# Performance work log

Hardware: AMD Instinct MI355X
Metric: run time of the kernel (lower is better)

The kernel has to match this reference:

```python
import jax, jax.numpy as jnp
import numpy as np

B, EMBED, HIDDEN, NH, D, H, W = 8, 384, 512, 32, 12, 32, 32  # attn_size D = EMBED // NH
SCALE = float(D) ** -0.5


def conv1x1(x, Wm, b):
    # 1x1 conv == per-pixel linear: x (B,Cin,H,W), Wm (Cout,Cin), b (Cout,)
    return jnp.einsum('bchw,oc->bohw', x, Wm) + b[None, :, None, None]


def mha(qc, kc, vc):
    # qc/kc/vc: (B, EMBED, H, W); tokens = H*W, heads = NH, head_dim = D
    HW = H * W
    def split(t):
        return t.reshape(B, NH, D, HW).transpose(0, 1, 3, 2)  # (B, nh, HW, d)
    q = split(qc) * SCALE
    k = split(kc)
    v = split(vc)
    w = jax.nn.softmax(jnp.einsum('bhnd,bhmd->bhnm', q, k), axis=-1)  # (B,nh,HW,HW)
    f = jnp.einsum('bhnm,bhmd->bhnd', w, v)  # (B,nh,HW,d)
    # (B,nh,HW,d) -> (B,HW,nh,d) -> (B,H,W,C) -> (B,C,H,W), matching torch view
    return f.transpose(0, 2, 1, 3).reshape(B, H, W, NH * D).transpose(0, 3, 1, 2)


def setup_inputs() -> dict:
    key = jax.random.key(0)
    ks = jax.random.split(key, 18)
    def p(k, shape):
        return jax.random.normal(k, shape, dtype=jnp.float32) * 0.02
    return {
        'x': jax.random.normal(ks[0], (B, EMBED, H, W), dtype=jnp.float32),
        'x_bpf': jax.random.normal(ks[1], (B, EMBED, H, W), dtype=jnp.float32),
        'Wq': p(ks[2], (EMBED, EMBED)), 'bq': p(ks[3], (EMBED,)),
        'Wk': p(ks[4], (EMBED, EMBED)), 'bk': p(ks[5], (EMBED,)),
        'Wv': p(ks[6], (EMBED, EMBED)), 'bv': p(ks[7], (EMBED,)),
        'Wq_bpf': p(ks[8], (EMBED, EMBED)), 'bq_bpf': p(ks[9], (EMBED,)),
        'Wk_bpf': p(ks[10], (EMBED, EMBED)), 'bk_bpf': p(ks[11], (EMBED,)),
        'Wv_bpf': p(ks[12], (EMBED, EMBED)), 'bv_bpf': p(ks[13], (EMBED,)),
        'Wo': p(ks[14], (HIDDEN, 2 * EMBED)), 'bo': p(ks[15], (HIDDEN,)),
    }


def reference(x, x_bpf, Wq, bq, Wk, bk, Wv, bv, Wq_bpf, bq_bpf, Wk_bpf, bk_bpf, Wv_bpf, bv_bpf, Wo, bo):
    q = conv1x1(x, Wq, bq)
    k = conv1x1(x, Wk, bk)
    v = conv1x1(x, Wv, bv)
    q_bpf = conv1x1(x_bpf, Wq_bpf, bq_bpf)
    k_bpf = conv1x1(x_bpf, Wk_bpf, bk_bpf)
    v_bpf = conv1x1(x_bpf, Wv_bpf, bv_bpf)
    # branch 1: query from bpf stream, key/value from x stream, residual to x
    f = mha(q_bpf, k, v) + x
    # branch 2: query from x stream, key/value from bpf stream, residual to x_bpf
    f_bpf = mha(q, k_bpf, v_bpf) + x_bpf
    fused = jnp.concatenate([f, f_bpf], axis=1)  # (B, 2*EMBED, H, W)
    return conv1x1(fused, Wo, bo)  # (B, HIDDEN, H, W)
```

## Files before the change

kernel.cpp:

```cpp
#include <hip/hip_runtime.h>
#include <hip/hip_bf16.h>

#define BB 8
#define EMBED 384
#define NH 32
#define HD 12
#define HWN 1024
#define HIDDEN 512
#define KTOT 1536
#define SCALE 0.28867513459481287f

typedef __attribute__((ext_vector_type(8))) unsigned short ushort8;
typedef __attribute__((ext_vector_type(8))) short short8;
typedef __attribute__((ext_vector_type(4))) float f32x4;
typedef __attribute__((ext_vector_type(16))) float f32x16;
typedef __attribute__((ext_vector_type(4))) unsigned short ushort4v;
typedef __attribute__((ext_vector_type(2))) unsigned int uint2v;

static __device__ __forceinline__ float bf2f(unsigned short u) {
    return __uint_as_float(((unsigned int)u) << 16);
}
static __device__ __forceinline__ unsigned short f2bf(float f) {
    unsigned int u = __float_as_uint(f);
    u = u + 0x7FFFu + ((u >> 16) & 1u);
    return (unsigned short)(u >> 16);
}
static __device__ __forceinline__ unsigned int cvt_pk_bf16(float lo, float hi) {
    unsigned int r;
    asm("v_cvt_pk_bf16_f32 %0, %1, %2" : "=v"(r) : "v"(lo), "v"(hi));
    return r;
}

struct WConv {
    const float* src[7];
    unsigned short* dst[7];
    int start[8];
};

__global__ __launch_bounds__(256) void k_bf16_all(WConv wc) {
    int i = blockIdx.x * 256 + threadIdx.x;
    if (i >= wc.start[7]) return;
    int p = 0;
#pragma unroll
    for (int j = 1; j < 7; ++j) p += (i >= wc.start[j]);
    const int e = i - wc.start[p];
    const f32x4 v = reinterpret_cast<const f32x4*>(wc.src[p])[e];
    ushort4v o;
#pragma unroll
    for (int j = 0; j < 4; ++j) o[j] = f2bf(v[j]);
    if (p == 6) {
        const int row = e / 192, cc = e % 192;
        ushort4v* d = reinterpret_cast<ushort4v*>(wc.dst[6]);
        d[row * 384 + cc] = o;
        d[row * 384 + 192 + cc] = o;
    } else {
        reinterpret_cast<ushort4v*>(wc.dst[p])[e] = o;
    }
}

__global__ __launch_bounds__(256) void k_transpose(const float* __restrict__ x0, const float* __restrict__ x1,
                                                   unsigned short* __restrict__ fused2) {
    __shared__ float tile[32][33];
    const int z = blockIdx.z;
    const int s = z >> 3, b = z & 7;
    const float* src = (s ? x1 : x0) + (size_t)b * EMBED * HWN;
    unsigned short* dst = fused2 + (size_t)b * HWN * KTOT + 768 + s * 384;
    const int c0 = blockIdx.x * 32;
    const int n0 = blockIdx.y * 32;
    const int tc = threadIdx.x & 31;
    const int tr = threadIdx.x >> 5;
#pragma unroll
    for (int p = 0; p < 4; ++p) {
        int r = tr + p * 8;
        tile[r][tc] = src[(size_t)(c0 + r) * HWN + n0 + tc];
    }
    __syncthreads();
#pragma unroll
    for (int p = 0; p < 4; ++p) {
        int r = tr + p * 8;
        dst[(size_t)(n0 + r) * KTOT + c0 + tc] = f2bf(tile[tc][r]);
    }
}

template <bool F32OUT>
static __device__ __forceinline__ void gemm_core(const unsigned short* __restrict__ A, int lda,
                                                 const unsigned short* __restrict__ Bt, int ldb,
                                                 const float* __restrict__ bias,
                                                 unsigned short* __restrict__ outBf,
                                                 float* __restrict__ outF,
                                                 int K, int bx, int by) {
    __shared__ unsigned short As[64][72];
    __shared__ unsigned short Bs[64][72];
    const int t = threadIdx.x;
    const int lane = t & 63;
    const int wid = t >> 6;
    const int wr = wid >> 1, wc = wid & 1;
    const int o0 = bx * 64, n0 = by * 64;
    const int lrow = t >> 2;
    const int lseg = t & 3;

    f32x4 acc[2][2] = {};

    for (int k0 = 0; k0 < K; k0 += 64) {
        const ushort8* ga = reinterpret_cast<const ushort8*>(A + (size_t)(o0 + lrow) * lda + k0 + lseg * 16);
        const ushort8* gb = reinterpret_cast<const ushort8*>(Bt + (size_t)(n0 + lrow) * ldb + k0 + lseg * 16);
        ushort8 a0 = ga[0], a1 = ga[1];
        ushort8 b0 = gb[0], b1 = gb[1];
        *reinterpret_cast<ushort8*>(&As[lrow][lseg * 16]) = a0;
        *reinterpret_cast<ushort8*>(&As[lrow][lseg * 16 + 8]) = a1;
        *reinterpret_cast<ushort8*>(&Bs[lrow][lseg * 16]) = b0;
        *reinterpret_cast<ushort8*>(&Bs[lrow][lseg * 16 + 8]) = b1;
        __syncthreads();
#pragma unroll
        for (int kk = 0; kk < 2; ++kk) {
            const int ko = kk * 32 + ((lane >> 4) << 3);
            short8 af[2], bfv[2];
            af[0]  = *reinterpret_cast<const short8*>(&As[wr * 32 + (lane & 15)][ko]);
            af[1]  = *reinterpret_cast<const short8*>(&As[wr * 32 + 16 + (lane & 15)][ko]);
            bfv[0] = *reinterpret_cast<const short8*>(&Bs[wc * 32 + (lane & 15)][ko]);
            bfv[1] = *reinterpret_cast<const short8*>(&Bs[wc * 32 + 16 + (lane & 15)][ko]);
#pragma unroll
            for (int i = 0; i < 2; ++i)
#pragma unroll
                for (int j = 0; j < 2; ++j)
                    acc[i][j] = __builtin_amdgcn_mfma_f32_16x16x32_bf16(af[i], bfv[j], acc[i][j], 0, 0, 0);
        }
        __syncthreads();
    }
#pragma unroll
    for (int i = 0; i < 2; ++i) {
#pragma unroll
        for (int j = 0; j < 2; ++j) {
            const int ob = o0 + wr * 32 + i * 16 + ((lane >> 4) << 2);
            const int n  = n0 + wc * 32 + j * 16 + (lane & 15);
#pragma unroll
            for (int r = 0; r < 4; ++r) {
                const int o = ob + r;
                float v = acc[i][j][r] + bias[o];
                if constexpr (F32OUT) outF[(size_t)o * HWN + n] = v;
                else                  outBf[(size_t)o * HWN + n] = f2bf(v);
            }
        }
    }
}

struct QkvTable {
    const unsigned short* W[6];
    const float* bias[6];
    const unsigned short* fused2;
    unsigned short* out[6];
};

__global__ __launch_bounds__(256) void k_gemm_qkv(QkvTable tab) {
    const int z = blockIdx.z;
    const int b = z / 6, p = z % 6;
    const unsigned short* Bt = tab.fused2 + (size_t)b * HWN * KTOT + 768 + (p / 3) * 384;
    gemm_core<false>(tab.W[p], EMBED, Bt, KTOT, tab.bias[p],
                     tab.out[p] + (size_t)b * EMBED * HWN, nullptr,
                     EMBED, blockIdx.x, blockIdx.y);
}

__global__ __launch_bounds__(256) void k_gemm_out(const unsigned short* __restrict__ Wo2,
                                                  const unsigned short* __restrict__ fused2,
                                                  const float* __restrict__ bo,
                                                  float* __restrict__ out) {
    const int b = blockIdx.z;
    gemm_core<true>(Wo2, KTOT, fused2 + (size_t)b * HWN * KTOT, KTOT, bo,
                    nullptr, out + (size_t)b * HIDDEN * HWN,
                    KTOT, blockIdx.x, blockIdx.y);
}

__global__ __launch_bounds__(256) void k_attn_mfma(const unsigned short* __restrict__ qc,
                                                   const unsigned short* __restrict__ kc,
                                                   const unsigned short* __restrict__ vc,
                                                   const unsigned short* __restrict__ qcb,
                                                   const unsigned short* __restrict__ kcb,
                                                   const unsigned short* __restrict__ vcb,
                                                   unsigned short* __restrict__ fused2) {
    __shared__ unsigned short Ks[512][18];
    __shared__ unsigned short Vs[13][520];

    const int bid = blockIdx.x;
    const int inst = bid >> 3, qt = bid & 7;
    const int branch = inst >> 8, b = (inst >> 5) & 7, h = inst & 31;
    const unsigned short* Qg = branch ? qc : qcb;
    const unsigned short* Kg = branch ? kcb : kc;
    const unsigned short* Vg = branch ? vcb : vc;
    const int coff = branch ? 384 : 0;
    const size_t base = ((size_t)b * EMBED + h * HD) * HWN;
    const int t = threadIdx.x;
    const int lane = t & 63, w = t >> 6;
    const int q31 = lane & 31, hi = lane >> 5;
    const int n0 = qt * 128;
    const float C2 = SCALE * 1.4426950408889634f;

    short8 qf = {};
    {
        const int qg = n0 + w * 32 + q31;
#pragma unroll
        for (int j = 0; j < 8; ++j) {
            const int d = hi * 8 + j;
            if (d < HD)
                qf[j] = (short)f2bf(bf2f(Qg[base + (size_t)d * HWN + qg]) * C2);
        }
    }

    f32x16 acc, z16;
#pragma unroll
    for (int r = 0; r < 16; ++r) { acc[r] = 0.f; z16[r] = 0.f; }
    const int vrow = (q31 < HD) ? q31 : 12;

    for (int phase = 0; phase < 2; ++phase) {
        const int m0 = phase << 9;
        __syncthreads();
        {
            const size_t kb = base + (size_t)(4 * w) * HWN + m0;
#pragma unroll
            for (int it = 0; it < 8; ++it) {
                const int m = it * 64 + lane;
                unsigned int da = 0, db = 0;
                if (w < 3) {
                    da = (unsigned int)Kg[kb + m] | ((unsigned int)Kg[kb + HWN + m] << 16);
                    db = (unsigned int)Kg[kb + 2 * HWN + m] | ((unsigned int)Kg[kb + 3 * HWN + m] << 16);
                }
                unsigned int* p = reinterpret_cast<unsigned int*>(&Ks[m][w * 4]);
                p[0] = da;
                p[1] = db;
            }
        }
        if (w < 3) {
#pragma unroll
            for (int r = 0; r < 4; ++r) {
                const int d = 4 * w + r;
                *reinterpret_cast<ushort8*>(&Vs[d][lane * 8]) =
                    *reinterpret_cast<const ushort8*>(&Vg[base + (size_t)d * HWN + m0 + lane * 8]);
            }
        } else {
            ushort8 ones;
#pragma unroll
            for (int j = 0; j < 8; ++j) ones[j] = 0x3F80;
            *reinterpret_cast<ushort8*>(&Vs[12][lane * 8]) = ones;
        }
        __syncthreads();

        for (int mc = 0; mc < 16; ++mc) {
            const int mb = mc << 5;
            union { short8 v; unsigned int u[4]; } kf;
            {
                const unsigned int* kp = reinterpret_cast<const unsigned int*>(&Ks[mb + q31][hi * 8]);
                kf.u[0] = kp[0]; kf.u[1] = kp[1]; kf.u[2] = kp[2]; kf.u[3] = kp[3];
            }
            union { short8 v; uint2v u2[2]; } vf1, vf2;
            vf1.u2[0] = *reinterpret_cast<const uint2v*>(&Vs[vrow][mb + hi * 4]);
            vf1.u2[1] = *reinterpret_cast<const uint2v*>(&Vs[vrow][mb + 8 + hi * 4]);
            vf2.u2[0] = *reinterpret_cast<const uint2v*>(&Vs[vrow][mb + 16 + hi * 4]);
            vf2.u2[1] = *reinterpret_cast<const uint2v*>(&Vs[vrow][mb + 24 + hi * 4]);
            const f32x16 s = __builtin_amdgcn_mfma_f32_32x32x16_bf16(kf.v, qf, z16, 0, 0, 0);
            union { short8 v; unsigned int u[4]; } p1, p2;
#pragma unroll
            for (int r = 0; r < 4; ++r) {
                p1.u[r] = cvt_pk_bf16(__builtin_amdgcn_exp2f(s[2 * r]),
                                      __builtin_amdgcn_exp2f(s[2 * r + 1]));
                p2.u[r] = cvt_pk_bf16(__builtin_amdgcn_exp2f(s[8 + 2 * r]),
                                      __builtin_amdgcn_exp2f(s[8 + 2 * r + 1]));
            }
            acc = __builtin_amdgcn_mfma_f32_32x32x16_bf16(p1.v, vf1.v, acc, 0, 0, 0);
            acc = __builtin_amdgcn_mfma_f32_32x32x16_bf16(p2.v, vf2.v, acc, 0, 0, 0);
        }
    }

    float invq[16];
#pragma unroll
    for (int r = 0; r < 16; ++r)
        invq[r] = 1.0f / __shfl(acc[r], (lane & 32) | 12);

    __syncthreads();
    unsigned short* OtW = &Ks[0][0] + w * 384;
    if (q31 < HD) {
#pragma unroll
        for (int r2 = 0; r2 < 8; ++r2) {
            const int r = 2 * r2;
            const int q = (r & 3) + 8 * (r >> 2) + 4 * hi;
            const unsigned int dw = (unsigned int)f2bf(acc[r] * invq[r]) |
                                    ((unsigned int)f2bf(acc[r + 1] * invq[r + 1]) << 16);
            *reinterpret_cast<unsigned int*>(&OtW[q31 * 32 + q]) = dw;
        }
    }
    __syncthreads();
    {
        const int q = t >> 1, half = t & 1;
        const unsigned short* Osrc = &Ks[0][0] + (q >> 5) * 384 + (half * 6) * 32 + (q & 31);
        const unsigned int w0 = (unsigned int)Osrc[0]   | ((unsigned int)Osrc[32]  << 16);
        const unsigned int w1 = (unsigned int)Osrc[64]  | ((unsigned int)Osrc[96]  << 16);
        const unsigned int w2 = (unsigned int)Osrc[128] | ((unsigned int)Osrc[160] << 16);
        unsigned int* dst = reinterpret_cast<unsigned int*>(
            fused2 + ((size_t)b * HWN + n0 + q) * KTOT + coff + h * HD + half * 6);
        dst[0] = w0; dst[1] = w1; dst[2] = w2;
    }
}

extern "C" void kernel_launch(void* const* d_in, const int* in_sizes, int n_in,
                              void* d_out, int out_size, void* d_ws, size_t ws_size,
                              hipStream_t stream) {
    (void)in_sizes; (void)n_in; (void)out_size; (void)ws_size;
    const float* x   = (const float*)d_in[0];
    const float* xbp = (const float*)d_in[1];
    const float* Wq  = (const float*)d_in[2];  const float* bq  = (const float*)d_in[3];
    const float* Wk  = (const float*)d_in[4];  const float* bk  = (const float*)d_in[5];
    const float* Wv  = (const float*)d_in[6];  const float* bv  = (const float*)d_in[7];
    const float* Wqb = (const float*)d_in[8];  const float* bqb = (const float*)d_in[9];
    const float* Wkb = (const float*)d_in[10]; const float* bkb = (const float*)d_in[11];
    const float* Wvb = (const float*)d_in[12]; const float* bvb = (const float*)d_in[13];
    const float* Wo  = (const float*)d_in[14]; const float* bo  = (const float*)d_in[15];
    float* out = (float*)d_out;

    char* ws = (char*)d_ws;
    size_t off = 0;
    auto alloc = [&](size_t bytes) -> void* {
        void* p = ws + off;
        off = (off + bytes + 255) & ~(size_t)255;
        return p;
    };
    unsigned short* wbf[6];
    for (int i = 0; i < 6; ++i) wbf[i] = (unsigned short*)alloc((size_t)EMBED * EMBED * 2);
    unsigned short* wo2 = (unsigned short*)alloc((size_t)HIDDEN * KTOT * 2);
    unsigned short* qkv[6];
    for (int i = 0; i < 6; ++i) qkv[i] = (unsigned short*)alloc((size_t)BB * EMBED * HWN * 2);
    unsigned short* fused2 = (unsigned short*)alloc((size_t)BB * HWN * KTOT * 2);

    WConv wc;
    const float* wsrc[7] = {Wq, Wk, Wv, Wqb, Wkb, Wvb, Wo};
    unsigned short* wdst[7] = {wbf[0], wbf[1], wbf[2], wbf[3], wbf[4], wbf[5], wo2};
    int acc4 = 0;
    for (int i = 0; i < 7; ++i) {
        const int n = (i < 6) ? EMBED * EMBED : HIDDEN * 768;
        wc.src[i] = wsrc[i];
        wc.dst[i] = wdst[i];
        wc.start[i] = acc4;
        acc4 += n / 4;
    }
    wc.start[7] = acc4;
    k_bf16_all<<<(acc4 + 255) / 256, 256, 0, stream>>>(wc);

    k_transpose<<<dim3(EMBED / 32, HWN / 32, 16), 256, 0, stream>>>(x, xbp, fused2);

    QkvTable tab;
    tab.W[0] = wbf[0]; tab.W[1] = wbf[1]; tab.W[2] = wbf[2];
    tab.W[3] = wbf[3]; tab.W[4] = wbf[4]; tab.W[5] = wbf[5];
    tab.bias[0] = bq; tab.bias[1] = bk; tab.bias[2] = bv;
    tab.bias[3] = bqb; tab.bias[4] = bkb; tab.bias[5] = bvb;
    tab.fused2 = fused2;
    for (int i = 0; i < 6; ++i) tab.out[i] = qkv[i];
    k_gemm_qkv<<<dim3(EMBED / 64, HWN / 64, BB * 6), 256, 0, stream>>>(tab);

    k_attn_mfma<<<dim3(4096), 256, 0, stream>>>(qkv[0], qkv[1], qkv[2], qkv[3], qkv[4], qkv[5],
                                                fused2);

    k_gemm_out<<<dim3(HIDDEN / 64, HWN / 64, BB), 256, 0, stream>>>(wo2, fused2, bo, out);
}
```

Measured before the change: 166.4 us.

## Process two query tiles per attention block to reuse staged K/V

Each attention block now handles 256 queries instead of 128 by keeping two Q fragments and two accumulators per wave. The K/V tiles staged in shared memory are reused across both, which halves the total K/V global loads and staging work, and the grid drops from 4096 to 2048 blocks. Block indexing is also reordered so consecutive blocks map to different head instances rather than query tiles of the same head. The cost is higher register pressure, possibly lower occupancy, and fewer blocks to spread across the GPU. The output transpose staging uses a padded stride so eight sub-tiles fit in the existing shared buffer.

```diff
diff --git a/kernel.cpp b/kernel.cpp
--- a/kernel.cpp
+++ b/kernel.cpp
@@ -170,6 +170,7 @@
                     KTOT, blockIdx.x, blockIdx.y);
 }
 
+#define OT_STRIDE 416
 __global__ __launch_bounds__(256) void k_attn_mfma(const unsigned short* __restrict__ qc,
                                                    const unsigned short* __restrict__ kc,
                                                    const unsigned short* __restrict__ vc,
@@ -181,7 +182,7 @@
     __shared__ unsigned short Vs[13][520];
 
     const int bid = blockIdx.x;
-    const int inst = bid >> 3, qt = bid & 7;
+    const int inst = bid & 511, qt = bid >> 9;
     const int branch = inst >> 8, b = (inst >> 5) & 7, h = inst & 31;
     const unsigned short* Qg = branch ? qc : qcb;
     const unsigned short* Kg = branch ? kcb : kc;
@@ -191,23 +192,24 @@
     const int t = threadIdx.x;
     const int lane = t & 63, w = t >> 6;
     const int q31 = lane & 31, hi = lane >> 5;
-    const int n0 = qt * 128;
+    const int n0 = qt * 256;
     const float C2 = SCALE * 1.4426950408889634f;
 
-    short8 qf = {};
-    {
-        const int qg = n0 + w * 32 + q31;
+    short8 qf[2] = {};
+#pragma unroll
+    for (int i = 0; i < 2; ++i) {
+        const int qg = n0 + i * 128 + w * 32 + q31;
 #pragma unroll
         for (int j = 0; j < 8; ++j) {
             const int d = hi * 8 + j;
             if (d < HD)
-                qf[j] = (short)f2bf(bf2f(Qg[base + (size_t)d * HWN + qg]) * C2);
-        }
-    }
-
-    f32x16 acc, z16;
-#pragma unroll
-    for (int r = 0; r < 16; ++r) { acc[r] = 0.f; z16[r] = 0.f; }
+                qf[i][j] = (short)f2bf(bf2f(Qg[base + (size_t)d * HWN + qg]) * C2);
+        }
+    }
+
+    f32x16 acc[2], z16;
+#pragma unroll
+    for (int r = 0; r < 16; ++r) { acc[0][r] = 0.f; acc[1][r] = 0.f; z16[r] = 0.f; }
     const int vrow = (q31 < HD) ? q31 : 12;
 
     for (int phase = 0; phase < 2; ++phase) {
@@ -255,47 +257,59 @@
             vf1.u2[1] = *reinterpret_cast<const uint2v*>(&Vs[vrow][mb + 8 + hi * 4]);
             vf2.u2[0] = *reinterpret_cast<const uint2v*>(&Vs[vrow][mb + 16 + hi * 4]);
             vf2.u2[1] = *reinterpret_cast<const uint2v*>(&Vs[vrow][mb + 24 + hi * 4]);
-            const f32x16 s = __builtin_amdgcn_mfma_f32_32x32x16_bf16(kf.v, qf, z16, 0, 0, 0);
-            union { short8 v; unsigned int u[4]; } p1, p2;
-#pragma unroll
-            for (int r = 0; r < 4; ++r) {
-                p1.u[r] = cvt_pk_bf16(__builtin_amdgcn_exp2f(s[2 * r]),
-                                      __builtin_amdgcn_exp2f(s[2 * r + 1]));
-                p2.u[r] = cvt_pk_bf16(__builtin_amdgcn_exp2f(s[8 + 2 * r]),
-                                      __builtin_amdgcn_exp2f(s[8 + 2 * r + 1]));
-            }
-            acc = __builtin_amdgcn_mfma_f32_32x32x16_bf16(p1.v, vf1.v, acc, 0, 0, 0);
-            acc = __builtin_amdgcn_mfma_f32_32x32x16_bf16(p2.v, vf2.v, acc, 0, 0, 0);
-        }
-    }
-
-    float invq[16];
-#pragma unroll
-    for (int r = 0; r < 16; ++r)
-        invq[r] = 1.0f / __shfl(acc[r], (lane & 32) | 12);
+#pragma unroll
+            for (int i = 0; i < 2; ++i) {
+                const f32x16 s = __builtin_amdgcn_mfma_f32_32x32x16_bf16(kf.v, qf[i], z16, 0, 0, 0);
+                union { short8 v; unsigned int u[4]; } p1, p2;
+#pragma unroll
+                for (int r = 0; r < 4; ++r) {
+                    p1.u[r] = cvt_pk_bf16(__builtin_amdgcn_exp2f(s[2 * r]),
+                                          __builtin_amdgcn_exp2f(s[2 * r + 1]));
+                    p2.u[r] = cvt_pk_bf16(__builtin_amdgcn_exp2f(s[8 + 2 * r]),
+                                          __builtin_amdgcn_exp2f(s[8 + 2 * r + 1]));
+                }
+                acc[i] = __builtin_amdgcn_mfma_f32_32x32x16_bf16(p1.v, vf1.v, acc[i], 0, 0, 0);
+                acc[i] = __builtin_amdgcn_mfma_f32_32x32x16_bf16(p2.v, vf2.v, acc[i], 0, 0, 0);
+            }
+        }
+    }
+
+    float invq[2][16];
+#pragma unroll
+    for (int i = 0; i < 2; ++i)
+#pragma unroll
+        for (int r = 0; r < 16; ++r)
+            invq[i][r] = 1.0f / __shfl(acc[i][r], (lane & 32) | 12);
 
     __syncthreads();
-    unsigned short* OtW = &Ks[0][0] + w * 384;
-    if (q31 < HD) {
-#pragma unroll
-        for (int r2 = 0; r2 < 8; ++r2) {
-            const int r = 2 * r2;
-            const int q = (r & 3) + 8 * (r >> 2) + 4 * hi;
-            const unsigned int dw = (unsigned int)f2bf(acc[r] * invq[r]) |
-                                    ((unsigned int)f2bf(acc[r + 1] * invq[r + 1]) << 16);
-            *reinterpret_cast<unsigned int*>(&OtW[q31 * 32 + q]) = dw;
+#pragma unroll
+    for (int i = 0; i < 2; ++i) {
+        unsigned short* OtW = &Ks[0][0] + (i * 4 + w) * OT_STRIDE;
+        if (q31 < HD) {
+#pragma unroll
+            for (int r2 = 0; r2 < 8; ++r2) {
+                const int r = 2 * r2;
+                const int q = (r & 3) + 8 * (r >> 2) + 4 * hi;
+                const unsigned int dw = (unsigned int)f2bf(acc[i][r] * invq[i][r]) |
+                                        ((unsigned int)f2bf(acc[i][r + 1] * invq[i][r + 1]) << 16);
+                *reinterpret_cast<unsigned int*>(&OtW[q31 * 32 + q]) = dw;
+            }
         }
     }
     __syncthreads();
     {
-        const int q = t >> 1, half = t & 1;
-        const unsigned short* Osrc = &Ks[0][0] + (q >> 5) * 384 + (half * 6) * 32 + (q & 31);
-        const unsigned int w0 = (unsigned int)Osrc[0]   | ((unsigned int)Osrc[32]  << 16);
-        const unsigned int w1 = (unsigned int)Osrc[64]  | ((unsigned int)Osrc[96]  << 16);
-        const unsigned int w2 = (unsigned int)Osrc[128] | ((unsigned int)Osrc[160] << 16);
+        const int q = t;
+        const int obi = ((q >> 7) * 4) + ((q >> 5) & 3);
+        const int ql = q & 31;
+        const unsigned short* Osrc = &Ks[0][0] + obi * OT_STRIDE + ql;
+        unsigned int dwv[6];
+#pragma unroll
+        for (int dp = 0; dp < 6; ++dp)
+            dwv[dp] = (unsigned int)Osrc[(2 * dp) * 32] | ((unsigned int)Osrc[(2 * dp + 1) * 32] << 16);
         unsigned int* dst = reinterpret_cast<unsigned int*>(
-            fused2 + ((size_t)b * HWN + n0 + q) * KTOT + coff + h * HD + half * 6);
-        dst[0] = w0; dst[1] = w1; dst[2] = w2;
+            fused2 + ((size_t)b * HWN + n0 + q) * KTOT + coff + h * HD);
+#pragma unroll
+        for (int dp = 0; dp < 6; ++dp) dst[dp] = dwv[dp];
     }
 }
 
@@ -353,7 +367,7 @@
     for (int i = 0; i < 6; ++i) tab.out[i] = qkv[i];
     k_gemm_qkv<<<dim3(EMBED / 64, HWN / 64, BB * 6), 256, 0, stream>>>(tab);
 
-    k_attn_mfma<<<dim3(4096), 256, 0, stream>>>(qkv[0], qkv[1], qkv[2], qkv[3], qkv[4], qkv[5],
+    k_attn_mfma<<<dim3(2048), 256, 0, stream>>>(qkv[0], qkv[1], qkv[2], qkv[3], qkv[4], qkv[5],
                                                 fused2);
 
     k_gemm_out<<<dim3(HIDDEN / 64, HWN / 64, BB), 256, 0, stream>>>(wo2, fused2, bo, out);
```

Measured after the change: 177.3 us. 1.07x slower.
